# Kernel optimization log

Measured on AMD Instinct MI355X. Metric: run time of the kernel, lower is better.

Reference implementation:

```python
import jax, jax.numpy as jnp
import numpy as np

B, L, D = 32, 256, 512
MAX_DUR = 8.0
MAX_LEN = int(L * MAX_DUR)  # static upper bound on expanded length (round(u<8) <= 8)


def setup_inputs() -> dict:
    key = jax.random.key(0)
    k1, k2 = jax.random.split(key)
    att_out = jax.random.normal(k1, (B, L, D), dtype=jnp.float32)
    # predicted per-phoneme durations in frames (float, gets rounded inside)
    duration = jax.random.uniform(k2, (B, L), dtype=jnp.float32, minval=0.0, maxval=MAX_DUR)
    return {"att_out": att_out, "duration": duration, "alpha": 1}


def reference(att_out, duration, alpha):
    # r[b,l] = number of times phoneme l is repeated (torch.round = half-to-even, same as jnp.round)
    r = jnp.round(duration * alpha).astype(jnp.int32)                 # [B, L]
    csum = jnp.cumsum(r, axis=1)                                      # [B, L] cumulative end offsets
    total = csum[:, -1]                                               # [B] valid length per batch
    pos = jnp.arange(MAX_LEN, dtype=jnp.int32)                        # [T]
    # output frame t comes from phoneme index = first l with csum[l] > t
    idx = jax.vmap(lambda c: jnp.searchsorted(c, pos, side='right'))(csum)  # [B, T]
    idx = jnp.minimum(idx, L - 1)
    out = jnp.take_along_axis(att_out, idx[:, :, None], axis=1)       # [B, T, D] gather-expand
    mask = (pos[None, :] < total[:, None])[:, :, None]                # zero-pad like pad_sequence
    return jnp.where(mask, out, jnp.zeros((), dtype=att_out.dtype))
```

## Files before the change

### kernel.cpp

```cpp
#include <hip/hip_runtime.h>


constexpr int B = 32;
constexpr int L = 256;
constexpr int D = 512;
constexpr int MAX_LEN = 2048;
constexpr int POS = 32;
constexpr int THREADS = 256;

typedef float fvec4 __attribute__((ext_vector_type(4)));

__global__ __launch_bounds__(THREADS) void length_regulator_kernel(
    const float* __restrict__ att_out,
    const float* __restrict__ duration,
    const int*   __restrict__ alpha_p,
    float*       __restrict__ out)
{
    __shared__ int csum[L];
    __shared__ int idx_tab[POS];
    __shared__ int wsum[4];

    const int tid  = threadIdx.x;
    const int lane = tid & 63;
    const int wave = tid >> 6;

    const int lin      = blockIdx.y * gridDim.x + blockIdx.x;
    const int xcd      = lin & 7;
    const int slot     = lin >> 3;
    const int b        = xcd * (B / 8) + (slot >> 6);
    const int pos_base = (slot & 63) * POS;

    const float alpha = (float)alpha_p[0];

    int x = (int)rintf(duration[b * L + tid] * alpha);
    #pragma unroll
    for (int off = 1; off < 64; off <<= 1) {
        int y = __shfl_up(x, off);
        x += (lane >= off) ? y : 0;
    }
    if (lane == 63) wsum[wave] = x;
    __syncthreads();
    const int w0 = wsum[0], w1 = wsum[1], w2 = wsum[2], w3 = wsum[3];
    const int total = w0 + w1 + w2 + w3;
    const int woff = (wave > 0 ? w0 : 0) + (wave > 1 ? w1 : 0) + (wave > 2 ? w2 : 0);
    csum[tid] = x + woff;
    __syncthreads();

    const int lane_r = tid & 127;
    const int rowsel = tid >> 7;

    fvec4* __restrict__ dst4 =
        (fvec4*)(out + ((size_t)b * MAX_LEN + pos_base) * D);

    if (pos_base >= total) {
        const fvec4 z = (fvec4){0.f, 0.f, 0.f, 0.f};
        #pragma unroll
        for (int i = 0; i < POS; i += 2) {
            __builtin_nontemporal_store(
                z, &dst4[(size_t)(i + rowsel) * (D / 4) + lane_r]);
        }
        return;
    }

    if (tid < POS) {
        const int p = pos_base + tid;
        int lo = 0;
        #pragma unroll
        for (int step = 128; step >= 1; step >>= 1) {
            const int nxt = lo + step;
            if (nxt <= L && csum[nxt - 1] <= p) lo = nxt;
        }
        idx_tab[tid] = min(lo, L - 1);
    }
    __syncthreads();

    const fvec4* __restrict__ src4 = (const fvec4*)(att_out + (size_t)b * L * D);

    fvec4 v[POS / 2];
    #pragma unroll
    for (int i = 0; i < POS; i += 2) {
        const int srow = idx_tab[i + rowsel];
        v[i / 2] = src4[(size_t)srow * (D / 4) + lane_r];
    }
    __builtin_amdgcn_sched_barrier(0);

    if (pos_base + POS <= total) {
        #pragma unroll
        for (int i = 0; i < POS; i += 2) {
            __builtin_nontemporal_store(
                v[i / 2], &dst4[(size_t)(i + rowsel) * (D / 4) + lane_r]);
        }
    } else {
        #pragma unroll
        for (int i = 0; i < POS; i += 2) {
            const int rp = i + rowsel;
            const bool keep = (pos_base + rp) < total;
            const fvec4 t = v[i / 2];
            const fvec4 val = keep ? t : (fvec4){0.f, 0.f, 0.f, 0.f};
            __builtin_nontemporal_store(
                val, &dst4[(size_t)rp * (D / 4) + lane_r]);
        }
    }
}

extern "C" void kernel_launch(void* const* d_in, const int* in_sizes, int n_in,
                              void* d_out, int out_size, void* d_ws, size_t ws_size,
                              hipStream_t stream) {
    const float* att_out  = (const float*)d_in[0];
    const float* duration = (const float*)d_in[1];
    const int*   alpha    = (const int*)d_in[2];
    float*       out      = (float*)d_out;

    dim3 grid(MAX_LEN / POS, B);
    dim3 block(THREADS);
    length_regulator_kernel<<<grid, block, 0, stream>>>(att_out, duration, alpha, out);
}
```

Measured before the change: 159.2 us.

## Split index computation into a precompute kernel and simplify copy kernel

Moves the duration rounding, prefix sum and binary search into a separate per-batch kernel that writes the gather indices and totals to workspace. The copy kernel then only loads 32 indices per block instead of redoing the full 256-element scan for each of the 2048 blocks. It also replaces nontemporal stores with plain stores and drops the batched-load/sched_barrier structure. The cost is an extra kernel launch plus a serial dependency on it, and possibly less memory-level parallelism and worse cache behaviour on stores.

```diff
diff --git a/kernel.cpp b/kernel.cpp
--- a/kernel.cpp
+++ b/kernel.cpp
@@ -10,25 +10,19 @@
 
 typedef float fvec4 __attribute__((ext_vector_type(4)));
 
-__global__ __launch_bounds__(THREADS) void length_regulator_kernel(
-    const float* __restrict__ att_out,
+__global__ __launch_bounds__(THREADS) void idx_precompute_kernel(
     const float* __restrict__ duration,
     const int*   __restrict__ alpha_p,
-    float*       __restrict__ out)
+    int*         __restrict__ ws_idx,
+    int*         __restrict__ ws_total)
 {
     __shared__ int csum[L];
-    __shared__ int idx_tab[POS];
     __shared__ int wsum[4];
 
+    const int b    = blockIdx.x;
     const int tid  = threadIdx.x;
     const int lane = tid & 63;
     const int wave = tid >> 6;
-
-    const int lin      = blockIdx.y * gridDim.x + blockIdx.x;
-    const int xcd      = lin & 7;
-    const int slot     = lin >> 3;
-    const int b        = xcd * (B / 8) + (slot >> 6);
-    const int pos_base = (slot & 63) * POS;
 
     const float alpha = (float)alpha_p[0];
 
@@ -41,10 +35,41 @@
     if (lane == 63) wsum[wave] = x;
     __syncthreads();
     const int w0 = wsum[0], w1 = wsum[1], w2 = wsum[2], w3 = wsum[3];
-    const int total = w0 + w1 + w2 + w3;
     const int woff = (wave > 0 ? w0 : 0) + (wave > 1 ? w1 : 0) + (wave > 2 ? w2 : 0);
     csum[tid] = x + woff;
     __syncthreads();
+    if (tid == 0) ws_total[b] = w0 + w1 + w2 + w3;
+
+    #pragma unroll
+    for (int k = 0; k < MAX_LEN / THREADS; ++k) {
+        const int p = k * THREADS + tid;
+        int lo = 0;
+        #pragma unroll
+        for (int step = 128; step >= 1; step >>= 1) {
+            const int nxt = lo + step;
+            if (nxt <= L && csum[nxt - 1] <= p) lo = nxt;
+        }
+        ws_idx[b * MAX_LEN + p] = min(lo, L - 1);
+    }
+}
+
+__global__ __launch_bounds__(THREADS) void length_regulator_copy_kernel(
+    const float* __restrict__ att_out,
+    const int*   __restrict__ ws_idx,
+    const int*   __restrict__ ws_total,
+    float*       __restrict__ out)
+{
+    __shared__ int s_idx[POS];
+
+    const int tid = threadIdx.x;
+
+    const int lin      = blockIdx.y * gridDim.x + blockIdx.x;
+    const int xcd      = lin & 7;
+    const int slot     = lin >> 3;
+    const int b        = xcd * (B / 8) + (slot >> 6);
+    const int pos_base = (slot & 63) * POS;
+
+    const int total = ws_total[b];
 
     const int lane_r = tid & 127;
     const int rowsel = tid >> 7;
@@ -55,51 +80,24 @@
     if (pos_base >= total) {
         const fvec4 z = (fvec4){0.f, 0.f, 0.f, 0.f};
         #pragma unroll
-        for (int i = 0; i < POS; i += 2) {
-            __builtin_nontemporal_store(
-                z, &dst4[(size_t)(i + rowsel) * (D / 4) + lane_r]);
-        }
+        for (int i = 0; i < POS; i += 2)
+            dst4[(size_t)(i + rowsel) * (D / 4) + lane_r] = z;
         return;
     }
 
-    if (tid < POS) {
-        const int p = pos_base + tid;
-        int lo = 0;
-        #pragma unroll
-        for (int step = 128; step >= 1; step >>= 1) {
-            const int nxt = lo + step;
-            if (nxt <= L && csum[nxt - 1] <= p) lo = nxt;
-        }
-        idx_tab[tid] = min(lo, L - 1);
-    }
+    if (tid < POS) s_idx[tid] = ws_idx[b * MAX_LEN + pos_base + tid];
     __syncthreads();
 
     const fvec4* __restrict__ src4 = (const fvec4*)(att_out + (size_t)b * L * D);
 
-    fvec4 v[POS / 2];
     #pragma unroll
     for (int i = 0; i < POS; i += 2) {
-        const int srow = idx_tab[i + rowsel];
-        v[i / 2] = src4[(size_t)srow * (D / 4) + lane_r];
-    }
-    __builtin_amdgcn_sched_barrier(0);
-
-    if (pos_base + POS <= total) {
-        #pragma unroll
-        for (int i = 0; i < POS; i += 2) {
-            __builtin_nontemporal_store(
-                v[i / 2], &dst4[(size_t)(i + rowsel) * (D / 4) + lane_r]);
-        }
-    } else {
-        #pragma unroll
-        for (int i = 0; i < POS; i += 2) {
-            const int rp = i + rowsel;
-            const bool keep = (pos_base + rp) < total;
-            const fvec4 t = v[i / 2];
-            const fvec4 val = keep ? t : (fvec4){0.f, 0.f, 0.f, 0.f};
-            __builtin_nontemporal_store(
-                val, &dst4[(size_t)rp * (D / 4) + lane_r]);
-        }
+        const int rp   = i + rowsel;
+        const int srow = s_idx[rp];
+        fvec4 t = src4[(size_t)srow * (D / 4) + lane_r];
+        const bool keep = (pos_base + rp) < total;
+        const fvec4 val = keep ? t : (fvec4){0.f, 0.f, 0.f, 0.f};
+        dst4[(size_t)rp * (D / 4) + lane_r] = val;
     }
 }
 
@@ -111,7 +109,13 @@
     const int*   alpha    = (const int*)d_in[2];
     float*       out      = (float*)d_out;
 
+    int* ws_idx   = (int*)d_ws;
+    int* ws_total = ws_idx + B * MAX_LEN;
+
+    idx_precompute_kernel<<<dim3(B), dim3(THREADS), 0, stream>>>(
+        duration, alpha, ws_idx, ws_total);
+
     dim3 grid(MAX_LEN / POS, B);
-    dim3 block(THREADS);
-    length_regulator_kernel<<<grid, block, 0, stream>>>(att_out, duration, alpha, out);
+    length_regulator_copy_kernel<<<grid, dim3(THREADS), 0, stream>>>(
+        att_out, ws_idx, ws_total, out);
 }
```

New measurement: 160.3 us. Within noise of the previous version (+0.7%).
